# Performance work log

Hardware: AMD Instinct MI355X
Metric: run time of the kernel (lower is better)

## Reference

```python
import jax, jax.numpy as jnp
import numpy as np

P_SIZE = 13
B_THRESH = 1.3  # |u| >= b -> hard 1.0
N_POW = 64      # u^n / (u^n + 1)


def make_dct_weight(p):
    idx = np.arange(p)
    Ci = np.where(idx == 0, 1.0 / np.sqrt(2.0), 1.0)
    cos = np.cos((2 * idx[:, None] + 1) * idx[None, :] * np.pi / (2 * p)) * Ci[None, :]  # [x,i]
    P = (2.0 / p) * np.einsum('xi,yj->xyij', cos, cos).reshape(p * p, p * p)
    return P.T.astype(np.float32).reshape(p * p, 1, p, p)


def conv2d(x, w, padding):
    return jax.lax.conv_general_dilated(x, w, (1, 1), padding,
                                        dimension_numbers=('NCHW', 'OIHW', 'NCHW'))


def udiff(u):
    # x^64/(x^64+1), saturated to 1 for |x| >= 1.3 (even power, sign-safe)
    au = jnp.abs(u)
    us = jnp.where(au < B_THRESH, u, 0.0)  # avoid overflow in pow
    y = us ** N_POW
    return jnp.where(au >= B_THRESH, jnp.ones_like(u), y / (y + 1.0))


def setup_inputs() -> dict:
    key = jax.random.key(0)
    k1, _ = jax.random.split(key)
    x = jax.random.uniform(k1, (2, 1, 512, 512), dtype=jnp.float32)
    sigma = jnp.full((1,), 0.1, dtype=jnp.float32)
    W_dct = jnp.asarray(make_dct_weight(P_SIZE))  # [p^2, 1, p, p], learnable in original
    return {"x": x, "sigma": sigma, "W_dct": W_dct}


def reference(x, sigma, W_dct):
    N, _, H, W = x.shape
    p = W_dct.shape[-1]
    pp = p * p
    # patch DCT: [N, p^2, H-p+1, W-p+1]
    t = conv2d(x, W_dct, 'VALID')
    nz = udiff(t / (3.0 * sigma))
    y = t * nz
    w = 1.0 / (1.0 + jnp.sum(nz, axis=1, keepdims=True))  # [N,1,H',W']
    # inverse transform as 1x1 conv with inv(dct matrix)
    Minv = jnp.linalg.inv(W_dct.reshape(pp, pp))
    z = jnp.einsum('kc,nchw->nkhw', Minv, y)
    z = w * z
    # overlap-add fold == conv with spatially-flipped identity patch kernel, full padding
    fold_k = jnp.flip(jnp.eye(pp, dtype=x.dtype).reshape(pp, p, p), axis=(1, 2))[None]  # [1,p^2,p,p]
    folded = conv2d(z, fold_k, [(p - 1, p - 1), (p - 1, p - 1)])  # [N,1,H,W]
    out = folded[:, :, p - 1:H - (p - 1), p - 1:W - (p - 1)]
    divisor = conv2d(w, jnp.ones((1, 1, p, p), x.dtype), 'VALID')
    return out / divisor
```

## Files before the change

### kernel.cpp

```cpp
#include <hip/hip_runtime.h>
#include <math.h>


#define P13    13
#define IMGW   512
#define OUTW   488
#define SEGH   31
#define NSEG   16
#define HCOLS  512
#define HPITCH 16

struct C1mat { float v[P13 * P13]; };

constexpr double kPI = 3.14159265358979323846264338327950288;

constexpr double ccos_pm_pi(double th) {
    double term = 1.0, s = 1.0;
    const double th2 = th * th;
    for (int n = 1; n <= 25; ++n) {
        term *= -th2 / (double)((2 * n - 1) * (2 * n));
        s += term;
    }
    return s;
}
constexpr double csqrt(double v) {
    double x = (v > 1.0) ? v : 1.0;
    for (int i = 0; i < 64; ++i) x = 0.5 * (x + v / x);
    return x;
}
constexpr C1mat make_c1() {
    C1mat m{};
    const double s213 = csqrt(2.0 / 13.0);
    const double is2  = 1.0 / csqrt(2.0);
    for (int x = 0; x < P13; ++x)
        for (int k = 0; k < P13; ++k) {
            int mm = ((2 * x + 1) * k) % 52;
            double th = (mm <= 26) ? (mm * kPI / 26.0) : ((mm - 52) * kPI / 26.0);
            double Ci = (k == 0) ? is2 : 1.0;
            m.v[x * P13 + k] = (float)(s213 * Ci * ccos_pm_pi(th));
        }
    return m;
}
__device__ constexpr C1mat c1c = make_c1();

struct CTab { int idx[P13][P13]; bool neg[P13][P13]; float a[14]; };
constexpr CTab make_ctab() {
    CTab t{};
    const double s213 = csqrt(2.0 / 13.0);
    for (int q = 0; q <= 12; ++q) t.a[q] = (float)(s213 * ccos_pm_pi(q * kPI / 26.0));
    t.a[13] = (float)(s213 / csqrt(2.0));
    for (int r = 0; r < P13; ++r)
        for (int c = 0; c < P13; ++c) {
            if (c == 0) { t.idx[r][c] = 13; t.neg[r][c] = false; continue; }
            int m = ((2 * r + 1) * c) % 52;
            int q; bool n;
            if (m <= 13)      { q = m;      n = false; }
            else if (m <= 26) { q = 26 - m; n = true;  }
            else if (m <= 39) { q = m - 26; n = true;  }
            else              { q = 52 - m; n = false; }
            t.idx[r][c] = q; t.neg[r][c] = n;
        }
    return t;
}
constexpr CTab ctab = make_ctab();

#define KC(r, c) (ctab.neg[(r)][(c)] ? -As[ctab.idx[(r)][(c)]] : As[ctab.idx[(r)][(c)]])

struct FalseT { static constexpr bool value = false; };
struct TrueT  { static constexpr bool value = true; };

#define ROR16_ADD(v, N)                                                        \
    v += __int_as_float(__builtin_amdgcn_mov_dpp(__float_as_int(v),            \
                                                 0x120 + (N), 0xF, 0xF, true))

__device__ __forceinline__ void vdct_shrink(const float (&Rv)[P13], const float (&As)[14],
                                            float i2sq, float (&tn)[P13], float& pnzr)
{
    float Se[6], So[6];
#pragma unroll
    for (int k = 0; k < 6; ++k) { Se[k] = Rv[k] + Rv[12 - k]; So[k] = Rv[k] - Rv[12 - k]; }
#pragma unroll
    for (int i = 0; i < P13; ++i) {
        float t;
        if ((i & 1) == 0) {
            t = KC(6, i) * Rv[6];
#pragma unroll
            for (int k = 0; k < 6; ++k) t = fmaf(KC(k, i), Se[k], t);
        } else {
            t = KC(0, i) * So[0];
#pragma unroll
            for (int k = 1; k < 6; ++k) t = fmaf(KC(k, i), So[k], t);
        }
        float p2 = fminf(t * t * i2sq, 1.69f);
        float p4 = p2 * p2, p8 = p4 * p4, p16 = p8 * p8, p32 = p16 * p16, p64 = p32 * p32;
        float r  = __builtin_amdgcn_rcpf(p64 + 1.0f);
        pnzr += r;
        tn[i] = fmaf(-t, r, t);
    }
}

__device__ __forceinline__ void fold_vert(const float (&tn)[P13], const float (&As)[14],
                                          float w1, float (&H)[P13])
{
#pragma unroll
    for (int dx = 0; dx < 6; ++dx) {
        float E = KC(dx, 0) * tn[0];
#pragma unroll
        for (int i = 2; i < P13; i += 2) E = fmaf(KC(dx, i), tn[i], E);
        float O = KC(dx, 1) * tn[1];
#pragma unroll
        for (int i = 3; i < P13; i += 2) O = fmaf(KC(dx, i), tn[i], O);
        H[dx]      = fmaf(w1, E + O, H[dx]);
        H[12 - dx] = fmaf(w1, E - O, H[12 - dx]);
    }
    float z6 = KC(6, 0) * tn[0];
#pragma unroll
    for (int i = 2; i < P13; i += 2) z6 = fmaf(KC(6, i), tn[i], z6);
    H[6] = fmaf(w1, z6, H[6]);
}

__global__ __launch_bounds__(256) void dct2net_k2(
    const float* __restrict__ xg, const float* __restrict__ sigmag,
    float* __restrict__ Hg, float* __restrict__ Wg)
{
    __shared__ float c1lds[169];
    const int tid = threadIdx.x;
    if (tid < 169) c1lds[tid] = c1c.v[tid];
    __syncthreads();

    const int lane = tid & 63;
    const int wv   = tid >> 6;
    const int g    = lane >> 4;
    const int jj   = lane & 15;
    const int img  = blockIdx.z;
    const int hs   = blockIdx.y * SEGH;
    const int segrows = (OUTW - hs < SEGH) ? (OUTW - hs) : SEGH;
    const int cbw  = blockIdx.x * 16 + wv * 4;
    const int col  = cbw + g;

    const float inv3s = 1.0f / (3.0f * sigmag[0]);
    const float i2sq  = inv3s * inv3s;
    const float* xin  = xg + (size_t)img * IMGW * IMGW;

    float As[14];
#pragma unroll
    for (int q = 0; q < 14; ++q) As[q] = ctab.a[q];
#pragma unroll
    for (int q = 0; q < 14; ++q) asm("" : "+s"(As[q]));

    float c1col[P13];
#pragma unroll
    for (int y = 0; y < P13; ++y)
        c1col[y] = (jj < 13) ? c1lds[y * P13 + jj] : 0.0f;

    float Rv[P13], Hr[P13], wr[12];
#pragma unroll
    for (int k = 0; k < P13; ++k) { Rv[k] = 0.0f; Hr[k] = 0.0f; }
#pragma unroll
    for (int k = 0; k < 12; ++k) wr[k] = 0.0f;
    float vs = 0.0f;

    int xcol = cbw + (lane & 15); xcol = (xcol < IMGW - 1) ? xcol : (IMGW - 1);
    const float* xp    = xin + (size_t)hs * IMGW;
    const float* xlast = xin + (size_t)(IMGW - 1) * IMGW;
    float xv = xp[xcol];
    xp += IMGW;

    float* Hp = Hg + ((size_t)img * OUTW + hs) * HCOLS * HPITCH;
    float* Wp = Wg + ((size_t)img * IMGW + hs) * IMGW;
    const int voH = col * HPITCH + jj;
    const int voW = col;

    auto step = [&](auto SH, auto RT) {
        float xw[P13];
#pragma unroll
        for (int y = 0; y < P13; ++y)
            xw[y] = __int_as_float(
                __builtin_amdgcn_ds_bpermute(4 * (g + y), __float_as_int(xv)));
        { const float* xq = (xp < xlast) ? xp : xlast; xv = xq[xcol]; xp += IMGW; }
        float a0 = c1col[0] * xw[0], a1 = c1col[1] * xw[1];
#pragma unroll
        for (int y = 2; y < P13; y += 2) a0 = fmaf(c1col[y], xw[y], a0);
#pragma unroll
        for (int y = 3; y < P13; y += 2) a1 = fmaf(c1col[y], xw[y], a1);
#pragma unroll
        for (int q = 0; q < P13 - 1; ++q) Rv[q] = Rv[q + 1];
        Rv[P13 - 1] = a0 + a1;

        if constexpr (decltype(SH)::value) {
            float tn[P13]; float pnzr = 0.0f;
            vdct_shrink(Rv, As, i2sq, tn, pnzr);
            float pnz = 13.0f - pnzr;
            ROR16_ADD(pnz, 1); ROR16_ADD(pnz, 2); ROR16_ADD(pnz, 4); ROR16_ADD(pnz, 8);
            const float w = __builtin_amdgcn_rcpf(1.0f + pnz);
            vs += w;
            fold_vert(tn, As, w, Hr);
            if constexpr (decltype(RT)::value) {
                Hp[voH] = Hr[0];
                Hp += HCOLS * HPITCH;
                if (jj == 0) Wp[voW] = vs;
                Wp += IMGW;
                vs -= wr[0];
            }
#pragma unroll
            for (int q = 0; q < 11; ++q) wr[q] = wr[q + 1];
            wr[11] = w;
#pragma unroll
            for (int q = 0; q < P13 - 1; ++q) Hr[q] = Hr[q + 1];
            Hr[P13 - 1] = 0.0f;
        }
    };

#pragma unroll 4
    for (int k = 0; k < 12; ++k) step(FalseT{}, FalseT{});
#pragma unroll 4
    for (int k = 0; k < 12; ++k) step(TrueT{}, FalseT{});
    const int kend = segrows;
#pragma unroll 4
    for (int k = 0; k < kend; ++k) step(TrueT{}, TrueT{});
}

__global__ __launch_bounds__(256) void dct2net_k3(
    const float* __restrict__ Hg, const float* __restrict__ Wg,
    float* __restrict__ outg)
{
    __shared__ float U[4][76][14];
    __shared__ float vw[4][80];
    const int tid  = threadIdx.x;
    const int lane = tid & 63;
    const int wv   = tid >> 6;
    const int img  = blockIdx.z;
    const int a0   = blockIdx.y * 4;
    const int a    = a0 + wv;
    const int cb   = blockIdx.x * 64;

    int c = cb + lane; c = (c < 499) ? c : 499;
    const float* hp = &Hg[(((size_t)img * OUTW + a) * HCOLS + c) * HPITCH];
    float4 m0 = *(const float4*)hp;
    float4 m1 = *(const float4*)(hp + 4);
    float4 m2 = *(const float4*)(hp + 8);
    float  m3 = hp[12];
    float  wm = Wg[((size_t)img * IMGW + a) * IMGW + c];

    const bool halo = (tid < 48);
    const int  hr = tid / 12;
    const int  hm = tid - hr * 12;
    float4 s0 = {0,0,0,0}, s1 = {0,0,0,0}, s2 = {0,0,0,0};
    float  s3 = 0.0f, ws = 0.0f;
    if (halo) {
        const int ah = a0 + hr;
        int c2 = cb + 64 + hm; c2 = (c2 < 499) ? c2 : 499;
        const float* hq = &Hg[(((size_t)img * OUTW + ah) * HCOLS + c2) * HPITCH];
        s0 = *(const float4*)hq;
        s1 = *(const float4*)(hq + 4);
        s2 = *(const float4*)(hq + 8);
        s3 = hq[12];
        ws = Wg[((size_t)img * IMGW + ah) * IMGW + c2];
    }

    {
        float hv[P13] = {m0.x,m0.y,m0.z,m0.w, m1.x,m1.y,m1.z,m1.w,
                         m2.x,m2.y,m2.z,m2.w, m3};
#pragma unroll
        for (int dy = 0; dy < P13; ++dy) {
            float u0 = c1c.v[dy * P13 + 0] * hv[0];
            float u1 = c1c.v[dy * P13 + 1] * hv[1];
#pragma unroll
            for (int j = 2; j < P13; j += 2) u0 = fmaf(c1c.v[dy * P13 + j], hv[j], u0);
#pragma unroll
            for (int j = 3; j < P13; j += 2) u1 = fmaf(c1c.v[dy * P13 + j], hv[j], u1);
            U[wv][lane][dy] = u0 + u1;
        }
        vw[wv][lane] = wm;
    }
    if (halo) {
        float hv[P13] = {s0.x,s0.y,s0.z,s0.w, s1.x,s1.y,s1.z,s1.w,
                         s2.x,s2.y,s2.z,s2.w, s3};
#pragma unroll
        for (int dy = 0; dy < P13; ++dy) {
            float u0 = c1c.v[dy * P13 + 0] * hv[0];
            float u1 = c1c.v[dy * P13 + 1] * hv[1];
#pragma unroll
            for (int j = 2; j < P13; j += 2) u0 = fmaf(c1c.v[dy * P13 + j], hv[j], u0);
#pragma unroll
            for (int j = 3; j < P13; j += 2) u1 = fmaf(c1c.v[dy * P13 + j], hv[j], u1);
            U[hr][64 + hm][dy] = u0 + u1;
        }
        vw[hr][64 + hm] = ws;
    }
    __syncthreads();

    float num = 0.0f;
#pragma unroll
    for (int dy = 0; dy < P13; ++dy) num += U[wv][lane + 12 - dy][dy];
    float den = 0.0f;
#pragma unroll
    for (int d = 0; d < P13; ++d) den += vw[wv][lane + d];
    const int ow = cb + lane;
    if (ow < OUTW)
        outg[((size_t)img * OUTW + a) * OUTW + ow] = num * __builtin_amdgcn_rcpf(den);
}

extern "C" void kernel_launch(void* const* d_in, const int* in_sizes, int n_in,
                              void* d_out, int out_size, void* d_ws, size_t ws_size,
                              hipStream_t stream)
{
    const float* x     = (const float*)d_in[0];
    const float* sigma = (const float*)d_in[1];
    float* out = (float*)d_out;

    float* Hg = (float*)d_ws;
    float* Wg = Hg + (size_t)2 * OUTW * HCOLS * HPITCH;

    dct2net_k2<<<dim3(32, NSEG, 2), 256, 0, stream>>>(x, sigma, Hg, Wg);
    dct2net_k3<<<dim3(8, 122, 2), 256, 0, stream>>>(Hg, Wg, out);
}
```

Measured before the change: 178.8 us.

## Replace sliding vertical DCT matvec with Chebyshev-style recurrence and fold sigma scaling

Instead of recomputing the full 13-point vertical DCT of the sliding window at every row, the kernel now updates each coefficient with a second-order cosine recurrence from the two previous outputs plus the entering and leaving samples. This cuts the per-row multiply-add count. The 1/(3 sigma) scale is folded into the row DCT coefficients and undone by multiplying by 3 sigma in the second kernel. The second kernel also builds its inverse column transform with symmetric even/odd sums. The recurrence accumulates float rounding error over each segment, and the row loops are no longer unrolled.

```diff
diff --git a/kernel.cpp b/kernel.cpp
--- a/kernel.cpp
+++ b/kernel.cpp
@@ -43,12 +43,13 @@
 }
 __device__ constexpr C1mat c1c = make_c1();
 
-struct CTab { int idx[P13][P13]; bool neg[P13][P13]; float a[14]; };
+struct CTab { int idx[P13][P13]; bool neg[P13][P13]; float a[14]; float b[6]; };
 constexpr CTab make_ctab() {
     CTab t{};
     const double s213 = csqrt(2.0 / 13.0);
     for (int q = 0; q <= 12; ++q) t.a[q] = (float)(s213 * ccos_pm_pi(q * kPI / 26.0));
     t.a[13] = (float)(s213 / csqrt(2.0));
+    for (int q = 0; q < 6; ++q) t.b[q] = (float)(2.0 * ccos_pm_pi((q + 1) * kPI / 13.0));
     for (int r = 0; r < P13; ++r)
         for (int c = 0; c < P13; ++c) {
             if (c == 0) { t.idx[r][c] = 13; t.neg[r][c] = false; continue; }
@@ -73,32 +74,6 @@
     v += __int_as_float(__builtin_amdgcn_mov_dpp(__float_as_int(v),            \
                                                  0x120 + (N), 0xF, 0xF, true))
 
-__device__ __forceinline__ void vdct_shrink(const float (&Rv)[P13], const float (&As)[14],
-                                            float i2sq, float (&tn)[P13], float& pnzr)
-{
-    float Se[6], So[6];
-#pragma unroll
-    for (int k = 0; k < 6; ++k) { Se[k] = Rv[k] + Rv[12 - k]; So[k] = Rv[k] - Rv[12 - k]; }
-#pragma unroll
-    for (int i = 0; i < P13; ++i) {
-        float t;
-        if ((i & 1) == 0) {
-            t = KC(6, i) * Rv[6];
-#pragma unroll
-            for (int k = 0; k < 6; ++k) t = fmaf(KC(k, i), Se[k], t);
-        } else {
-            t = KC(0, i) * So[0];
-#pragma unroll
-            for (int k = 1; k < 6; ++k) t = fmaf(KC(k, i), So[k], t);
-        }
-        float p2 = fminf(t * t * i2sq, 1.69f);
-        float p4 = p2 * p2, p8 = p4 * p4, p16 = p8 * p8, p32 = p16 * p16, p64 = p32 * p32;
-        float r  = __builtin_amdgcn_rcpf(p64 + 1.0f);
-        pnzr += r;
-        tn[i] = fmaf(-t, r, t);
-    }
-}
-
 __device__ __forceinline__ void fold_vert(const float (&tn)[P13], const float (&As)[14],
                                           float w1, float (&H)[P13])
 {
@@ -139,26 +114,29 @@
     const int col  = cbw + g;
 
     const float inv3s = 1.0f / (3.0f * sigmag[0]);
-    const float i2sq  = inv3s * inv3s;
     const float* xin  = xg + (size_t)img * IMGW * IMGW;
 
-    float As[14];
+    float As[14], Bs[6];
 #pragma unroll
     for (int q = 0; q < 14; ++q) As[q] = ctab.a[q];
 #pragma unroll
+    for (int q = 0; q < 6; ++q) Bs[q] = ctab.b[q];
+#pragma unroll
     for (int q = 0; q < 14; ++q) asm("" : "+s"(As[q]));
+#pragma unroll
+    for (int q = 0; q < 6; ++q) asm("" : "+s"(Bs[q]));
 
     float c1col[P13];
 #pragma unroll
     for (int y = 0; y < P13; ++y)
-        c1col[y] = (jj < 13) ? c1lds[y * P13 + jj] : 0.0f;
-
-    float Rv[P13], Hr[P13], wr[12];
-#pragma unroll
-    for (int k = 0; k < P13; ++k) { Rv[k] = 0.0f; Hr[k] = 0.0f; }
+        c1col[y] = (jj < 13) ? c1lds[y * P13 + jj] * inv3s : 0.0f;
+
+    float T0[P13], T1[P13], dr[P13], Hr[P13], wr[12], Rv[P13];
+#pragma unroll
+    for (int k = 0; k < P13; ++k) { T0[k]=0; T1[k]=0; dr[k]=0; Hr[k]=0; Rv[k]=0; }
 #pragma unroll
     for (int k = 0; k < 12; ++k) wr[k] = 0.0f;
-    float vs = 0.0f;
+    float vs = 0.0f, Rprev = 0.0f;
 
     int xcol = cbw + (lane & 15); xcol = (xcol < IMGW - 1) ? xcol : (IMGW - 1);
     const float* xp    = xin + (size_t)hs * IMGW;
@@ -171,7 +149,7 @@
     const int voH = col * HPITCH + jj;
     const int voW = col;
 
-    auto step = [&](auto SH, auto RT) {
+    auto front = [&]() -> float {
         float xw[P13];
 #pragma unroll
         for (int y = 0; y < P13; ++y)
@@ -183,46 +161,108 @@
         for (int y = 2; y < P13; y += 2) a0 = fmaf(c1col[y], xw[y], a0);
 #pragma unroll
         for (int y = 3; y < P13; y += 2) a1 = fmaf(c1col[y], xw[y], a1);
+        return a0 + a1;
+    };
+    auto pushRv = [&](float Rn) {
 #pragma unroll
         for (int q = 0; q < P13 - 1; ++q) Rv[q] = Rv[q + 1];
-        Rv[P13 - 1] = a0 + a1;
-
-        if constexpr (decltype(SH)::value) {
-            float tn[P13]; float pnzr = 0.0f;
-            vdct_shrink(Rv, As, i2sq, tn, pnzr);
-            float pnz = 13.0f - pnzr;
-            ROR16_ADD(pnz, 1); ROR16_ADD(pnz, 2); ROR16_ADD(pnz, 4); ROR16_ADD(pnz, 8);
-            const float w = __builtin_amdgcn_rcpf(1.0f + pnz);
-            vs += w;
-            fold_vert(tn, As, w, Hr);
-            if constexpr (decltype(RT)::value) {
-                Hp[voH] = Hr[0];
-                Hp += HCOLS * HPITCH;
-                if (jj == 0) Wp[voW] = vs;
-                Wp += IMGW;
-                vs -= wr[0];
+        Rv[P13 - 1] = Rn;
+    };
+    auto pushd = [&](float Rn) {
+        float dn = Rn - Rprev; Rprev = Rn;
+#pragma unroll
+        for (int q = 0; q < P13 - 1; ++q) dr[q] = dr[q + 1];
+        dr[P13 - 1] = dn;
+    };
+    auto matvec = [&](float (&T)[P13]) {
+        float Se[6], So[6];
+#pragma unroll
+        for (int k = 0; k < 6; ++k) { Se[k] = Rv[k] + Rv[12 - k]; So[k] = Rv[k] - Rv[12 - k]; }
+#pragma unroll
+        for (int i = 0; i < P13; ++i) {
+            float t;
+            if ((i & 1) == 0) {
+                t = KC(6, i) * Rv[6];
+#pragma unroll
+                for (int k = 0; k < 6; ++k) t = fmaf(KC(k, i), Se[k], t);
+            } else {
+                t = KC(0, i) * So[0];
+#pragma unroll
+                for (int k = 1; k < 6; ++k) t = fmaf(KC(k, i), So[k], t);
             }
-#pragma unroll
-            for (int q = 0; q < 11; ++q) wr[q] = wr[q + 1];
-            wr[11] = w;
-#pragma unroll
-            for (int q = 0; q < P13 - 1; ++q) Hr[q] = Hr[q + 1];
-            Hr[P13 - 1] = 0.0f;
-        }
-    };
-
-#pragma unroll 4
-    for (int k = 0; k < 12; ++k) step(FalseT{}, FalseT{});
-#pragma unroll 4
-    for (int k = 0; k < 12; ++k) step(TrueT{}, FalseT{});
-    const int kend = segrows;
-#pragma unroll 4
-    for (int k = 0; k < kend; ++k) step(TrueT{}, TrueT{});
+            T[i] = t;
+        }
+    };
+    auto sf = [&](const float (&T)[P13], bool rt) {
+        float tn[P13]; float pnzr = 0.0f;
+#pragma unroll
+        for (int i = 0; i < P13; ++i) {
+            float p2 = fminf(T[i] * T[i], 1.69f);
+            float p4 = p2 * p2, p8 = p4 * p4, p16 = p8 * p8, p32 = p16 * p16, p64 = p32 * p32;
+            float r  = __builtin_amdgcn_rcpf(p64 + 1.0f);
+            pnzr += r;
+            tn[i] = fmaf(-T[i], r, T[i]);
+        }
+        float pnz = 13.0f - pnzr;
+        ROR16_ADD(pnz, 1); ROR16_ADD(pnz, 2); ROR16_ADD(pnz, 4); ROR16_ADD(pnz, 8);
+        const float w = __builtin_amdgcn_rcpf(1.0f + pnz);
+        vs += w;
+        fold_vert(tn, As, w, Hr);
+        if (rt) {
+            Hp[voH] = Hr[0];
+            Hp += HCOLS * HPITCH;
+            if (jj == 0) Wp[voW] = vs;
+            Wp += IMGW;
+            vs -= wr[0];
+        }
+#pragma unroll
+        for (int q = 0; q < 11; ++q) wr[q] = wr[q + 1];
+        wr[11] = w;
+#pragma unroll
+        for (int q = 0; q < P13 - 1; ++q) Hr[q] = Hr[q + 1];
+        Hr[P13 - 1] = 0.0f;
+    };
+    auto recur = [&](auto INTOT0, bool rt) {
+        float Rn = front();
+        float dn = Rn - Rprev; Rprev = Rn;
+        float dl = dr[0];
+#pragma unroll
+        for (int q = 0; q < P13 - 1; ++q) dr[q] = dr[q + 1];
+        dr[P13 - 1] = dn;
+        float Pe = dn - dl, Po = dn + dl;
+#pragma unroll
+        for (int i = 0; i < P13; ++i) {
+            float tp2 = decltype(INTOT0)::value ? T0[i] : T1[i];
+            float tp1 = decltype(INTOT0)::value ? T1[i] : T0[i];
+            float c2 = (i == 0) ? 2.0f : ((i <= 6) ? Bs[i - 1] : -Bs[12 - i]);
+            float t = fmaf(c2, tp1, -tp2);
+            float kc = (i == 0) ? As[13] : As[i];
+            t = (i & 1) ? fmaf(-kc, Po, t) : fmaf(kc, Pe, t);
+            if constexpr (decltype(INTOT0)::value) T0[i] = t; else T1[i] = t;
+        }
+        if constexpr (decltype(INTOT0)::value) sf(T0, rt); else sf(T1, rt);
+    };
+
+    { float Rn = front(); Rprev = Rn; pushRv(Rn); }
+#pragma unroll 1
+    for (int k = 1; k < 12; ++k) { float Rn = front(); pushd(Rn); pushRv(Rn); }
+    { float Rn = front(); pushd(Rn); pushRv(Rn); matvec(T0); sf(T0, false); }
+    { float Rn = front(); pushd(Rn); pushRv(Rn); matvec(T1); sf(T1, false); }
+    {
+        int ks = 0; const int S = 10 + segrows;
+#pragma unroll 1
+        while (ks + 2 <= S) {
+            recur(TrueT{},  ks     >= 10);
+            recur(FalseT{}, ks + 1 >= 10);
+            ks += 2;
+        }
+        if (ks < S) recur(TrueT{}, ks >= 10);
+    }
 }
 
 __global__ __launch_bounds__(256) void dct2net_k3(
     const float* __restrict__ Hg, const float* __restrict__ Wg,
-    float* __restrict__ outg)
+    const float* __restrict__ sigmag, float* __restrict__ outg)
 {
     __shared__ float U[4][76][14];
     __shared__ float vw[4][80];
@@ -233,6 +273,14 @@
     const int a0   = blockIdx.y * 4;
     const int a    = a0 + wv;
     const int cb   = blockIdx.x * 64;
+
+    const float t3s = 3.0f * sigmag[0];
+
+    float As[14];
+#pragma unroll
+    for (int q = 0; q < 14; ++q) As[q] = ctab.a[q];
+#pragma unroll
+    for (int q = 0; q < 14; ++q) asm("" : "+s"(As[q]));
 
     int c = cb + lane; c = (c < 499) ? c : 499;
     const float* hp = &Hg[(((size_t)img * OUTW + a) * HCOLS + c) * HPITCH];
@@ -258,34 +306,32 @@
         ws = Wg[((size_t)img * IMGW + ah) * IMGW + c2];
     }
 
+    auto buildU = [&](const float (&hv)[P13], int uw, int uli) {
+#pragma unroll
+        for (int dy = 0; dy < 6; ++dy) {
+            float e = KC(dy, 0) * hv[0];
+#pragma unroll
+            for (int j = 2; j < P13; j += 2) e = fmaf(KC(dy, j), hv[j], e);
+            float o = KC(dy, 1) * hv[1];
+#pragma unroll
+            for (int j = 3; j < P13; j += 2) o = fmaf(KC(dy, j), hv[j], o);
+            U[uw][uli][dy]      = e + o;
+            U[uw][uli][12 - dy] = e - o;
+        }
+        float gsum = ((hv[4] - hv[2]) + (hv[8] - hv[6])) + (hv[12] - hv[10]);
+        U[uw][uli][6] = fmaf(As[0], gsum, As[13] * hv[0]);
+    };
+
     {
         float hv[P13] = {m0.x,m0.y,m0.z,m0.w, m1.x,m1.y,m1.z,m1.w,
                          m2.x,m2.y,m2.z,m2.w, m3};
-#pragma unroll
-        for (int dy = 0; dy < P13; ++dy) {
-            float u0 = c1c.v[dy * P13 + 0] * hv[0];
-            float u1 = c1c.v[dy * P13 + 1] * hv[1];
-#pragma unroll
-            for (int j = 2; j < P13; j += 2) u0 = fmaf(c1c.v[dy * P13 + j], hv[j], u0);
-#pragma unroll
-            for (int j = 3; j < P13; j += 2) u1 = fmaf(c1c.v[dy * P13 + j], hv[j], u1);
-            U[wv][lane][dy] = u0 + u1;
-        }
+        buildU(hv, wv, lane);
         vw[wv][lane] = wm;
     }
     if (halo) {
         float hv[P13] = {s0.x,s0.y,s0.z,s0.w, s1.x,s1.y,s1.z,s1.w,
                          s2.x,s2.y,s2.z,s2.w, s3};
-#pragma unroll
-        for (int dy = 0; dy < P13; ++dy) {
-            float u0 = c1c.v[dy * P13 + 0] * hv[0];
-            float u1 = c1c.v[dy * P13 + 1] * hv[1];
-#pragma unroll
-            for (int j = 2; j < P13; j += 2) u0 = fmaf(c1c.v[dy * P13 + j], hv[j], u0);
-#pragma unroll
-            for (int j = 3; j < P13; j += 2) u1 = fmaf(c1c.v[dy * P13 + j], hv[j], u1);
-            U[hr][64 + hm][dy] = u0 + u1;
-        }
+        buildU(hv, hr, 64 + hm);
         vw[hr][64 + hm] = ws;
     }
     __syncthreads();
@@ -298,7 +344,8 @@
     for (int d = 0; d < P13; ++d) den += vw[wv][lane + d];
     const int ow = cb + lane;
     if (ow < OUTW)
-        outg[((size_t)img * OUTW + a) * OUTW + ow] = num * __builtin_amdgcn_rcpf(den);
+        outg[((size_t)img * OUTW + a) * OUTW + ow] =
+            num * t3s * __builtin_amdgcn_rcpf(den);
 }
 
 extern "C" void kernel_launch(void* const* d_in, const int* in_sizes, int n_in,
@@ -313,5 +360,5 @@
     float* Wg = Hg + (size_t)2 * OUTW * HCOLS * HPITCH;
 
     dct2net_k2<<<dim3(32, NSEG, 2), 256, 0, stream>>>(x, sigma, Hg, Wg);
-    dct2net_k3<<<dim3(8, 122, 2), 256, 0, stream>>>(Hg, Wg, out);
-}
+    dct2net_k3<<<dim3(8, 122, 2), 256, 0, stream>>>(Hg, Wg, sigma, out);
+}
```

New measurement: 180.6 us. No clear change (+1.0%).
